# Kernel optimization log

Hardware: AMD Instinct MI355X
Metric: run time of the kernel (lower is better)

Reference implementation:

```python
import jax, jax.numpy as jnp
import numpy as np

DIM = 1024
HEADS = 16
HEAD_DIM = DIM // HEADS
SCALE = HEAD_DIM ** -0.5
EPS = 1e-5


def _ln(x, g, b):
    m = jnp.mean(x, axis=-1, keepdims=True)
    v = jnp.mean((x - m) ** 2, axis=-1, keepdims=True)
    return (x - m) * jax.lax.rsqrt(v + EPS) * g + b


def setup_inputs() -> dict:
    key = jax.random.key(0)
    ks = jax.random.split(key, 12)
    B, N, C = 4, 1024, DIM
    s = lambda fan: 1.0 / np.sqrt(fan)
    return {
        "src_q": jax.random.normal(ks[0], (B, N, C), jnp.float32),
        "src_kv": jax.random.normal(ks[1], (B, N, C), jnp.float32),
        "gq": jnp.ones((C,), jnp.float32), "bq": jnp.zeros((C,), jnp.float32),
        "gkv": jnp.ones((C,), jnp.float32), "bkv": jnp.zeros((C,), jnp.float32),
        "Wq": jax.random.normal(ks[2], (C, C), jnp.float32) * s(C),
        "Wkv": jax.random.normal(ks[3], (C, 2 * C), jnp.float32) * s(C),
        "Wproj": jax.random.normal(ks[4], (C, C), jnp.float32) * s(C),
        "bproj": jnp.zeros((C,), jnp.float32),
        "gn": jnp.ones((C,), jnp.float32), "bn": jnp.zeros((C,), jnp.float32),
        "W1": jax.random.normal(ks[5], (C, 4 * C), jnp.float32) * s(C),
        "b1": jnp.zeros((4 * C,), jnp.float32),
        "W2": jax.random.normal(ks[6], (4 * C, C), jnp.float32) * s(4 * C),
        "b2": jnp.zeros((C,), jnp.float32),
    }


def reference(src_q, src_kv, gq, bq, gkv, bkv, Wq, Wkv, Wproj, bproj,
              gn, bn, W1, b1, W2, b2):
    B, N, C = src_q.shape
    qn = _ln(src_q, gq, bq)
    kvn = _ln(src_kv, gkv, bkv)
    # Q: [B, H, N, d]
    Q = (qn @ Wq).reshape(B, N, HEADS, HEAD_DIM).transpose(0, 2, 1, 3)
    KV = (kvn @ Wkv).reshape(B, N, 2, HEADS, HEAD_DIM).transpose(2, 0, 3, 1, 4)
    K, V = KV[0], KV[1]
    attn = jnp.einsum('bhqd,bhkd->bhqk', Q, K) * SCALE
    attn = jax.nn.softmax(attn, axis=-1)
    # NOTE: original code multiplies by scale a second time here (faithful)
    x = jnp.einsum('bhqk,bhkd->bhqd', attn, V) * SCALE
    x = x.transpose(0, 2, 1, 3).reshape(B, N, C)
    x = x @ Wproj + bproj
    src = src_q + x               # residual (drop_path = identity in eval)
    src = _ln(src, gn, bn)
    h = jax.nn.gelu(src @ W1 + b1, approximate=False)
    src2 = h @ W2 + b2
    return src + src2
```

## Files before the change

### kernel.cpp

```cpp
#include <hip/hip_runtime.h>
#include <hip/hip_bf16.h>
#include <math.h>

typedef __bf16 bf16;
typedef __bf16 bf16x2 __attribute__((ext_vector_type(2)));
typedef __bf16 bf16x8 __attribute__((ext_vector_type(8)));
typedef float f32x4 __attribute__((ext_vector_type(4)));
typedef float f32x16 __attribute__((ext_vector_type(16)));
typedef unsigned int u32;
typedef unsigned int u32x2 __attribute__((ext_vector_type(2)));
typedef unsigned int u32x4 __attribute__((ext_vector_type(4)));

#define SCALE 0.125f

#define GLOAD_LDS16(gptr, lptr)                                      \
  __builtin_amdgcn_global_load_lds(                                  \
      (const __attribute__((address_space(1))) void*)(gptr),         \
      (__attribute__((address_space(3))) void*)(lptr), 16, 0, 0)

template <int N>
__device__ __forceinline__ void vmcnt_wait() {
  if constexpr (N == 0) asm volatile("s_waitcnt vmcnt(0)" ::: "memory");
  else if constexpr (N == 4) asm volatile("s_waitcnt vmcnt(4)" ::: "memory");
  else if constexpr (N == 6) asm volatile("s_waitcnt vmcnt(6)" ::: "memory");
  else static_assert(N == 0 || N == 4 || N == 6, "unsupported vmcnt");
}

__device__ __forceinline__ u32 pk_bf16(float lo, float hi) {
  bf16x2 t;
  t[0] = (bf16)lo;
  t[1] = (bf16)hi;
  return __builtin_bit_cast(u32, t);
}

__device__ __forceinline__ void plane32_swap(u32& a, u32& b) {
  asm volatile("v_permlane32_swap_b32 %0, %1" : "+v"(a), "+v"(b));
}

__global__ __launch_bounds__(256) void ln_f32(const float* __restrict__ x,
                                              const float* __restrict__ g,
                                              const float* __restrict__ b,
                                              bf16* __restrict__ y) {
  long base = (long)blockIdx.x * 1024;
  int tid = threadIdx.x;
  float v[4];
#pragma unroll
  for (int i = 0; i < 4; i++) v[i] = x[base + tid + i * 256];
  float s1 = v[0] + v[1] + v[2] + v[3];
  float s2 = v[0] * v[0] + v[1] * v[1] + v[2] * v[2] + v[3] * v[3];
#pragma unroll
  for (int off = 32; off; off >>= 1) {
    s1 += __shfl_xor(s1, off);
    s2 += __shfl_xor(s2, off);
  }
  __shared__ float aux[2][4];
  int wave = tid >> 6, lane = tid & 63;
  if (lane == 0) { aux[0][wave] = s1; aux[1][wave] = s2; }
  __syncthreads();
  float S1 = aux[0][0] + aux[0][1] + aux[0][2] + aux[0][3];
  float S2 = aux[1][0] + aux[1][1] + aux[1][2] + aux[1][3];
  float mean = S1 * (1.0f / 1024.0f);
  float var = S2 * (1.0f / 1024.0f) - mean * mean;
  float rs = rsqrtf(var + 1e-5f);
#pragma unroll
  for (int i = 0; i < 4; i++) {
    int c = tid + i * 256;
    y[base + c] = (bf16)(((v[i] - mean) * rs) * g[c] + b[c]);
  }
}

__global__ __launch_bounds__(256) void transpose_w(const float* __restrict__ W,
                                                   bf16* __restrict__ Wt,
                                                   int K, int N) {
  __shared__ bf16 tile[64][66];
  int n0 = blockIdx.x * 64, k0 = blockIdx.y * 64;
  int c = threadIdx.x & 63, r4 = threadIdx.x >> 6;
#pragma unroll
  for (int i = 0; i < 16; i++)
    tile[i * 4 + r4][c] = (bf16)W[(long)(k0 + i * 4 + r4) * N + n0 + c];
  __syncthreads();
#pragma unroll
  for (int i = 0; i < 16; i++)
    Wt[(long)(n0 + i * 4 + r4) * K + k0 + c] = tile[c][i * 4 + r4];
}

__global__ __launch_bounds__(256) void extract_vt(const bf16* __restrict__ KV,
                                                  bf16* __restrict__ Vt) {
  __shared__ bf16 tile[64][66];
  int bh = blockIdx.z, b = bh >> 4, h = bh & 15;
  const bf16* src = KV + (long)b * 1024 * 2048 + 1024 + h * 64;
  bf16* dst = Vt + (long)bh * 64 * 1024;
  int n0 = blockIdx.x * 64;
  int c = threadIdx.x & 63, r4 = threadIdx.x >> 6;
#pragma unroll
  for (int i = 0; i < 16; i++)
    tile[i * 4 + r4][c] = src[(long)(n0 + i * 4 + r4) * 2048 + c];
  __syncthreads();
#pragma unroll
  for (int i = 0; i < 16; i++)
    dst[(long)(i * 4 + r4) * 1024 + n0 + c] = tile[c][i * 4 + r4];
}

__global__ __launch_bounds__(256) void attn_fused(
    const bf16* __restrict__ Q,
    const bf16* __restrict__ KV,
    const bf16* __restrict__ Vt,
    bf16* __restrict__ X) {
  __shared__ __align__(16) bf16 Qs[128 * 64];
  __shared__ __align__(16) bf16 Ks[2][64 * 128];
  __shared__ __align__(16) bf16 Vs[2][64 * 128];
  int tid = threadIdx.x, wave = tid >> 6, lane = tid & 63;
  int l31 = lane & 31, h = lane >> 5;
  int bh = blockIdx.y, b = bh >> 4, hd = bh & 15;
  const bf16* Qb = Q + (long)b * 1048576 + hd * 64;
  const bf16* Kb = KV + (long)b * 2097152 + hd * 64;
  const bf16* Vb = Vt + (long)bh * 65536;
  bf16* Xb = X + (long)b * 1048576 + hd * 64;
  int q0 = blockIdx.x * 128;

  const bf16* gk[4];
  const bf16* gv[4];
  int eoKV[4];
#pragma unroll
  for (int t = 0; t < 4; t++) {
    int eo = (t * 256 + tid) * 8;
    eoKV[t] = eo;
    int r2 = eo >> 7, pp = (eo & 127) >> 3, q = pp ^ (r2 & 15);
    gk[t] = &Kb[(long)(r2 + ((q >> 3) << 6)) * 2048 + ((q & 7) << 3)];
    gv[t] = &Vb[(long)r2 * 1024 + (q << 3)];
  }

#pragma unroll
  for (int t = 0; t < 4; t++) {
    int eo = (t * 256 + tid) * 8;
    int r = eo >> 6, p = (eo & 63) >> 3;
    int c = (p ^ (r & 7)) << 3;
    GLOAD_LDS16(&Qb[(long)(q0 + r) * 1024 + c], &Qs[eo]);
  }
#pragma unroll
  for (int t = 0; t < 4; t++) GLOAD_LDS16(gk[t], &Ks[0][eoKV[t]]);
#pragma unroll
  for (int t = 0; t < 4; t++) GLOAD_LDS16(gv[t], &Vs[0][eoKV[t]]);
  __syncthreads();

  bf16x8 qf[4];
  {
    int r = wave * 32 + l31;
#pragma unroll
    for (int dw = 0; dw < 4; dw++) {
      int p = (dw * 2 + h) ^ (r & 7);
      qf[dw] = *(const bf16x8*)&Qs[r * 64 + p * 8];
    }
  }

  const float C = 0.18033688011112042f;
  float m_run = -1e30f, l_run = 0.0f;
  f32x16 acc[2] = {};
  int cur = 0;

  for (int kc = 0; kc < 8; kc++) {
    if (kc < 7) {
#pragma unroll
      for (int t = 0; t < 4; t++)
        GLOAD_LDS16(gk[t] + (long)(kc + 1) * 128 * 2048, &Ks[cur ^ 1][eoKV[t]]);
#pragma unroll
      for (int t = 0; t < 4; t++)
        GLOAD_LDS16(gv[t] + (kc + 1) * 128, &Vs[cur ^ 1][eoKV[t]]);
    }
    const bf16* ks = Ks[cur];
    const bf16* vs = Vs[cur];

    f32x16 s[4] = {};
#pragma unroll
    for (int kt = 0; kt < 4; kt++) {
      int k = kt * 32 + l31;
      int r2 = k & 63, hi = k >> 6;
#pragma unroll
      for (int dw = 0; dw < 4; dw++) {
        int p = (hi * 8 + dw * 2 + h) ^ (r2 & 15);
        bf16x8 kf = *(const bf16x8*)&ks[r2 * 128 + p * 8];
        s[kt] = __builtin_amdgcn_mfma_f32_32x32x16_bf16(kf, qf[dw], s[kt], 0, 0, 0);
      }
    }

    float mk[4];
#pragma unroll
    for (int kt = 0; kt < 4; kt++) {
      float m01 = fmaxf(fmaxf(s[kt][0], s[kt][1]), fmaxf(s[kt][2], s[kt][3]));
      float m23 = fmaxf(fmaxf(s[kt][4], s[kt][5]), fmaxf(s[kt][6], s[kt][7]));
      float m45 = fmaxf(fmaxf(s[kt][8], s[kt][9]), fmaxf(s[kt][10], s[kt][11]));
      float m67 = fmaxf(fmaxf(s[kt][12], s[kt][13]), fmaxf(s[kt][14], s[kt][15]));
      mk[kt] = fmaxf(fmaxf(m01, m23), fmaxf(m45, m67));
    }
    float mx = fmaxf(fmaxf(mk[0], mk[1]), fmaxf(mk[2], mk[3]));
    mx = fmaxf(mx, __shfl_xor(mx, 32));
    float m_new = fmaxf(m_run, mx);
    float alpha = exp2f((m_run - m_new) * C);
    m_run = m_new;
    float mc = m_new * C;
    float rk[4];
#pragma unroll
    for (int kt = 0; kt < 4; kt++) {
      float r0 = 0.0f;
#pragma unroll
      for (int r = 0; r < 16; r++) {
        float pv = exp2f(s[kt][r] * C - mc);
        s[kt][r] = pv;
        r0 += pv;
      }
      rk[kt] = r0;
    }
    float rs = (rk[0] + rk[1]) + (rk[2] + rk[3]);
    rs += __shfl_xor(rs, 32);
    l_run = l_run * alpha + rs;
#pragma unroll
    for (int nt = 0; nt < 2; nt++)
#pragma unroll
      for (int r = 0; r < 16; r++) acc[nt][r] *= alpha;

#pragma unroll
    for (int kw = 0; kw < 8; kw++) {
      int kt = kw >> 1, rb = (kw & 1) * 8;
      u32 wA = pk_bf16(s[kt][rb + 0], s[kt][rb + 1]);
      u32 wB = pk_bf16(s[kt][rb + 2], s[kt][rb + 3]);
      u32 wC = pk_bf16(s[kt][rb + 4], s[kt][rb + 5]);
      u32 wD = pk_bf16(s[kt][rb + 6], s[kt][rb + 7]);
      plane32_swap(wA, wC);
      plane32_swap(wB, wD);
      u32x4 wv = {wA, wB, wC, wD};
      bf16x8 pf = __builtin_bit_cast(bf16x8, wv);
#pragma unroll
      for (int nt = 0; nt < 2; nt++) {
        int r2 = nt * 32 + l31;
        int p = (kw * 2 + h) ^ (r2 & 15);
        bf16x8 vf = *(const bf16x8*)&vs[r2 * 128 + p * 8];
        acc[nt] = __builtin_amdgcn_mfma_f32_32x32x16_bf16(vf, pf, acc[nt], 0, 0, 0);
      }
    }

    if (kc < 7) {
      __syncthreads();
      cur ^= 1;
    }
  }

  float fs = SCALE / l_run;
  bf16* Os = Qs;
  int qrow = wave * 32 + l31;
#pragma unroll
  for (int nt = 0; nt < 2; nt++)
#pragma unroll
    for (int g = 0; g < 4; g++) {
      u32 w0 = pk_bf16(acc[nt][g * 4 + 0] * fs, acc[nt][g * 4 + 1] * fs);
      u32 w1 = pk_bf16(acc[nt][g * 4 + 2] * fs, acc[nt][g * 4 + 3] * fs);
      int s8 = nt * 8 + g * 2 + h;
      int phys = s8 ^ (qrow & 15);
      u32x2 wv = {w0, w1};
      *(u32x2*)&Os[qrow * 64 + phys * 4] = wv;
    }
  int rrow = wave * 32 + (lane >> 1);
  int cbase = (lane & 1) * 32;
#pragma unroll
  for (int t2 = 0; t2 < 4; t2++) {
    int s0 = (lane & 1) * 8 + t2 * 2;
    u32x2 a = *(u32x2*)&Os[rrow * 64 + ((s0 ^ (rrow & 15)) * 4)];
    u32x2 bb = *(u32x2*)&Os[rrow * 64 + (((s0 + 1) ^ (rrow & 15)) * 4)];
    u32x4 o4 = {a[0], a[1], bb[0], bb[1]};
    *(u32x4*)&Xb[(long)(q0 + rrow) * 1024 + cbase + t2 * 8] = o4;
  }
}

template <int BM, int BN, int WR, int WC, int PH, int EPI, int CF32, int RBF16>
__global__ __launch_bounds__(512) void gemm_p(
    const bf16* __restrict__ A, int lda,
    const bf16* __restrict__ B, int ldb,
    void* __restrict__ Cv, int ldc, int K,
    const float* __restrict__ bias,
    const void* __restrict__ resv, int ldr) {
  constexpr int MT = BM / (16 * WR);
  constexpr int NT = BN / (16 * WC);
  constexpr int KSP = 2 / PH;
  constexpr int L = (BM + BN) / 64;
  constexpr int LA = BM / 64;
  constexpr int AE = BM * 64;
  constexpr int BUFE = (BM + BN) * 64;
  __shared__ __align__(16) bf16 lds[3 * BUFE];
  int tid = threadIdx.x;
  int wave = tid >> 6, lane = tid & 63;
  int wm = wave / WC, wn = wave % WC;
  int quad = lane >> 4, l16 = lane & 15;
  int m0 = blockIdx.y * BM, n0 = blockIdx.x * BN;

  const bf16* gp[L];
  int lo[L];
#pragma unroll
  for (int i = 0; i < L; i++) {
    if (i < LA) {
      int eo = (i * 512 + tid) * 8;
      int r = eo >> 6, p = (eo & 63) >> 3;
      int c = (p ^ (r & 7)) << 3;
      gp[i] = &A[(long)(m0 + r) * lda + c];
      lo[i] = eo;
    } else {
      int eo = ((i - LA) * 512 + tid) * 8;
      int r = eo >> 6, p = (eo & 63) >> 3;
      int c = (p ^ (r & 7)) << 3;
      gp[i] = &B[(long)(n0 + r) * ldb + c];
      lo[i] = AE + eo;
    }
  }

  int ntk = K >> 6;
#pragma unroll
  for (int i = 0; i < L; i++) GLOAD_LDS16(gp[i], &lds[lo[i]]);
#pragma unroll
  for (int i = 0; i < L; i++) gp[i] += 64;
#pragma unroll
  for (int i = 0; i < L; i++) GLOAD_LDS16(gp[i], &lds[BUFE + lo[i]]);
#pragma unroll
  for (int i = 0; i < L; i++) gp[i] += 64;
  vmcnt_wait<L>();
  asm volatile("" ::: "memory");
  __builtin_amdgcn_s_barrier();

  f32x4 acc[MT][NT] = {};
  int b = 0;
  for (int t = 0; t < ntk; t++) {
    const bf16* Al = &lds[b * BUFE];
    const bf16* Bl = &lds[b * BUFE + AE];
    int b2 = b + 2; if (b2 >= 3) b2 -= 3;
    bool more = (t + 2) < ntk;
#pragma unroll
    for (int ph = 0; ph < PH; ph++) {
      bf16x8 af[KSP][MT], bv[KSP][NT];
#pragma unroll
      for (int k2 = 0; k2 < KSP; k2++) {
        int ks = ph * KSP + k2;
#pragma unroll
        for (int mt = 0; mt < MT; mt++) {
          int row = wm * (BM / WR) + mt * 16 + l16;
          int p = (ks * 4 + quad) ^ (row & 7);
          af[k2][mt] = *(const bf16x8*)&Al[row * 64 + p * 8];
        }
#pragma unroll
        for (int nt = 0; nt < NT; nt++) {
          int row = wn * (BN / WC) + nt * 16 + l16;
          int p = (ks * 4 + quad) ^ (row & 7);
          bv[k2][nt] = *(const bf16x8*)&Bl[row * 64 + p * 8];
        }
      }
      if (more) {
#pragma unroll
        for (int i = ph * L / PH; i < (ph + 1) * L / PH; i++)
          GLOAD_LDS16(gp[i], &lds[b2 * BUFE + lo[i]]);
      }
      if (ph == PH - 1) {
        if (more) vmcnt_wait<L>();
        else vmcnt_wait<0>();
      }
      asm volatile("" ::: "memory");
      __builtin_amdgcn_s_barrier();
      asm volatile("s_waitcnt lgkmcnt(0)" ::: "memory");
      __builtin_amdgcn_sched_barrier(0);
      __builtin_amdgcn_s_setprio(1);
#pragma unroll
      for (int k2 = 0; k2 < KSP; k2++)
#pragma unroll
        for (int mt = 0; mt < MT; mt++)
#pragma unroll
          for (int nt = 0; nt < NT; nt++)
            acc[mt][nt] = __builtin_amdgcn_mfma_f32_16x16x32_bf16(
                af[k2][mt], bv[k2][nt], acc[mt][nt], 0, 0, 0);
      __builtin_amdgcn_s_setprio(0);
      __builtin_amdgcn_sched_barrier(0);
      __builtin_amdgcn_s_barrier();
    }
#pragma unroll
    for (int i = 0; i < L; i++) gp[i] += 64;
    b += 1; if (b == 3) b = 0;
  }

  int gm = m0 + wm * (BM / WR), gn = n0 + wn * (BN / WC);
#pragma unroll
  for (int nt = 0; nt < NT; nt++) {
    int col = gn + nt * 16 + l16;
    float bvb = (EPI != 0) ? bias[col] : 0.0f;
#pragma unroll
    for (int mt = 0; mt < MT; mt++) {
#pragma unroll
      for (int r = 0; r < 4; r++) {
        int row = gm + mt * 16 + quad * 4 + r;
        float v = acc[mt][nt][r] + bvb;
        if (EPI == 2) {
          v = 0.5f * v * (1.0f + erff(v * 0.70710678118654752f));
        } else if (EPI == 1) {
          float rv = RBF16 ? (float)((const bf16*)resv)[(long)row * ldr + col]
                           : ((const float*)resv)[(long)row * ldr + col];
          v += rv;
        }
        if (CF32)
          ((float*)Cv)[(long)row * ldc + col] = v;
        else
          ((bf16*)Cv)[(long)row * ldc + col] = (bf16)v;
      }
    }
  }
}

extern "C" void kernel_launch(void* const* d_in, const int* in_sizes, int n_in,
                              void* d_out, int out_size, void* d_ws, size_t ws_size,
                              hipStream_t stream) {
  const float* src_q  = (const float*)d_in[0];
  const float* src_kv = (const float*)d_in[1];
  const float* gq     = (const float*)d_in[2];
  const float* bq     = (const float*)d_in[3];
  const float* gkv    = (const float*)d_in[4];
  const float* bkv    = (const float*)d_in[5];
  const float* Wq     = (const float*)d_in[6];
  const float* Wkv    = (const float*)d_in[7];
  const float* Wproj  = (const float*)d_in[8];
  const float* bproj  = (const float*)d_in[9];
  const float* gn     = (const float*)d_in[10];
  const float* bn     = (const float*)d_in[11];
  const float* W1     = (const float*)d_in[12];
  const float* b1     = (const float*)d_in[13];
  const float* W2     = (const float*)d_in[14];
  const float* b2     = (const float*)d_in[15];
  float* out = (float*)d_out;

  char* ws = (char*)d_ws;
  const long MB = 1024 * 1024;
  bf16* Wq_t    = (bf16*)(ws + 0 * MB);
  bf16* Wkv_t   = (bf16*)(ws + 2 * MB);
  bf16* Wproj_t = (bf16*)(ws + 6 * MB);
  bf16* W1_t    = (bf16*)(ws + 8 * MB);
  bf16* W2_t    = (bf16*)(ws + 16 * MB);
  bf16* qn      = (bf16*)(ws + 24 * MB);
  bf16* kvn     = (bf16*)(ws + 32 * MB);
  bf16* Qm      = (bf16*)(ws + 40 * MB);
  bf16* KVm     = (bf16*)(ws + 48 * MB);
  bf16* Vt      = (bf16*)(ws + 64 * MB);
  bf16* xbuf    = (bf16*)(ws + 24 * MB);
  float* tbuf   = (float*)(ws + 48 * MB);
  bf16* sbuf    = (bf16*)(ws + 64 * MB);
  bf16* hbuf    = (bf16*)(ws + 72 * MB);

  transpose_w<<<dim3(16, 16), 256, 0, stream>>>(Wq, Wq_t, 1024, 1024);
  transpose_w<<<dim3(32, 16), 256, 0, stream>>>(Wkv, Wkv_t, 1024, 2048);
  transpose_w<<<dim3(16, 16), 256, 0, stream>>>(Wproj, Wproj_t, 1024, 1024);
  transpose_w<<<dim3(64, 16), 256, 0, stream>>>(W1, W1_t, 1024, 4096);
  transpose_w<<<dim3(16, 64), 256, 0, stream>>>(W2, W2_t, 4096, 1024);

  ln_f32<<<4096, 256, 0, stream>>>(src_q, gq, bq, qn);
  ln_f32<<<4096, 256, 0, stream>>>(src_kv, gkv, bkv, kvn);

  gemm_p<128, 128, 2, 4, 1, 0, 0, 0><<<dim3(8, 32), 512, 0, stream>>>(
      qn, 1024, Wq_t, 1024, Qm, 1024, 1024, nullptr, nullptr, 0);
  gemm_p<256, 128, 4, 2, 2, 0, 0, 0><<<dim3(16, 16), 512, 0, stream>>>(
      kvn, 1024, Wkv_t, 1024, KVm, 2048, 1024, nullptr, nullptr, 0);
  extract_vt<<<dim3(16, 1, 64), 256, 0, stream>>>(KVm, Vt);

  attn_fused<<<dim3(8, 64), 256, 0, stream>>>(Qm, KVm, Vt, xbuf);

  gemm_p<128, 128, 2, 4, 1, 1, 1, 0><<<dim3(8, 32), 512, 0, stream>>>(
      xbuf, 1024, Wproj_t, 1024, tbuf, 1024, 1024, bproj, src_q, 1024);
  ln_f32<<<4096, 256, 0, stream>>>(tbuf, gn, bn, sbuf);
  gemm_p<256, 128, 4, 2, 2, 2, 0, 0><<<dim3(32, 16), 512, 0, stream>>>(
      sbuf, 1024, W1_t, 1024, hbuf, 4096, 1024, b1, nullptr, 0);
  gemm_p<128, 128, 2, 4, 1, 1, 1, 1><<<dim3(8, 32), 512, 0, stream>>>(
      hbuf, 4096, W2_t, 4096, out, 1024, 4096, b2, sbuf, 1024);
}
```

Baseline: 372.0 us.

## Restructure GEMM main loop to one barrier per k-tile and drop phase split

Removes the PH template parameter and its two-phase split of each k-tile. Every k-tile now reads both k-slices of fragments from LDS, issues all prefetch loads, runs the MFMAs, and only then waits on vmcnt and hits a single barrier. Before, each tile waited on vmcnt before compute and used two barriers. This cuts barrier count and lets the global-to-LDS prefetch overlap the MFMA block. In exchange, the larger tiles keep more fragment registers live and lose the finer interleaving of loads with compute.

```diff
diff --git a/kernel.cpp b/kernel.cpp
--- a/kernel.cpp
+++ b/kernel.cpp
@@ -270,7 +270,7 @@
   }
 }
 
-template <int BM, int BN, int WR, int WC, int PH, int EPI, int CF32, int RBF16>
+template <int BM, int BN, int WR, int WC, int EPI, int CF32, int RBF16>
 __global__ __launch_bounds__(512) void gemm_p(
     const bf16* __restrict__ A, int lda,
     const bf16* __restrict__ B, int ldb,
@@ -279,7 +279,6 @@
     const void* __restrict__ resv, int ldr) {
   constexpr int MT = BM / (16 * WR);
   constexpr int NT = BN / (16 * WC);
-  constexpr int KSP = 2 / PH;
   constexpr int L = (BM + BN) / 64;
   constexpr int LA = BM / 64;
   constexpr int AE = BM * 64;
@@ -330,49 +329,47 @@
     const bf16* Bl = &lds[b * BUFE + AE];
     int b2 = b + 2; if (b2 >= 3) b2 -= 3;
     bool more = (t + 2) < ntk;
-#pragma unroll
-    for (int ph = 0; ph < PH; ph++) {
-      bf16x8 af[KSP][MT], bv[KSP][NT];
-#pragma unroll
-      for (int k2 = 0; k2 < KSP; k2++) {
-        int ks = ph * KSP + k2;
-#pragma unroll
-        for (int mt = 0; mt < MT; mt++) {
-          int row = wm * (BM / WR) + mt * 16 + l16;
-          int p = (ks * 4 + quad) ^ (row & 7);
-          af[k2][mt] = *(const bf16x8*)&Al[row * 64 + p * 8];
-        }
-#pragma unroll
-        for (int nt = 0; nt < NT; nt++) {
-          int row = wn * (BN / WC) + nt * 16 + l16;
-          int p = (ks * 4 + quad) ^ (row & 7);
-          bv[k2][nt] = *(const bf16x8*)&Bl[row * 64 + p * 8];
-        }
-      }
-      if (more) {
-#pragma unroll
-        for (int i = ph * L / PH; i < (ph + 1) * L / PH; i++)
-          GLOAD_LDS16(gp[i], &lds[b2 * BUFE + lo[i]]);
-      }
-      if (ph == PH - 1) {
-        if (more) vmcnt_wait<L>();
-        else vmcnt_wait<0>();
-      }
+
+    bf16x8 af[2][MT], bv[2][NT];
+#pragma unroll
+    for (int ks = 0; ks < 2; ks++) {
+#pragma unroll
+      for (int mt = 0; mt < MT; mt++) {
+        int row = wm * (BM / WR) + mt * 16 + l16;
+        int p = (ks * 4 + quad) ^ (row & 7);
+        af[ks][mt] = *(const bf16x8*)&Al[row * 64 + p * 8];
+      }
+#pragma unroll
+      for (int nt = 0; nt < NT; nt++) {
+        int row = wn * (BN / WC) + nt * 16 + l16;
+        int p = (ks * 4 + quad) ^ (row & 7);
+        bv[ks][nt] = *(const bf16x8*)&Bl[row * 64 + p * 8];
+      }
+    }
+    if (more) {
+#pragma unroll
+      for (int i = 0; i < L; i++) GLOAD_LDS16(gp[i], &lds[b2 * BUFE + lo[i]]);
+    }
+    asm volatile("s_waitcnt lgkmcnt(0)" ::: "memory");
+    __builtin_amdgcn_sched_barrier(0);
+    __builtin_amdgcn_s_setprio(1);
+#pragma unroll
+    for (int ks = 0; ks < 2; ks++)
+#pragma unroll
+      for (int mt = 0; mt < MT; mt++)
+#pragma unroll
+        for (int nt = 0; nt < NT; nt++)
+          acc[mt][nt] = __builtin_amdgcn_mfma_f32_16x16x32_bf16(
+              af[ks][mt], bv[ks][nt], acc[mt][nt], 0, 0, 0);
+    __builtin_amdgcn_s_setprio(0);
+    __builtin_amdgcn_sched_barrier(0);
+    if (more) {
+      vmcnt_wait<L>();
+    } else if (t + 1 < ntk) {
+      vmcnt_wait<0>();
+    }
+    if (t + 1 < ntk) {
       asm volatile("" ::: "memory");
-      __builtin_amdgcn_s_barrier();
-      asm volatile("s_waitcnt lgkmcnt(0)" ::: "memory");
-      __builtin_amdgcn_sched_barrier(0);
-      __builtin_amdgcn_s_setprio(1);
-#pragma unroll
-      for (int k2 = 0; k2 < KSP; k2++)
-#pragma unroll
-        for (int mt = 0; mt < MT; mt++)
-#pragma unroll
-          for (int nt = 0; nt < NT; nt++)
-            acc[mt][nt] = __builtin_amdgcn_mfma_f32_16x16x32_bf16(
-                af[k2][mt], bv[k2][nt], acc[mt][nt], 0, 0, 0);
-      __builtin_amdgcn_s_setprio(0);
-      __builtin_amdgcn_sched_barrier(0);
       __builtin_amdgcn_s_barrier();
     }
 #pragma unroll
@@ -454,19 +451,19 @@
   ln_f32<<<4096, 256, 0, stream>>>(src_q, gq, bq, qn);
   ln_f32<<<4096, 256, 0, stream>>>(src_kv, gkv, bkv, kvn);
 
-  gemm_p<128, 128, 2, 4, 1, 0, 0, 0><<<dim3(8, 32), 512, 0, stream>>>(
+  gemm_p<128, 128, 2, 4, 0, 0, 0><<<dim3(8, 32), 512, 0, stream>>>(
       qn, 1024, Wq_t, 1024, Qm, 1024, 1024, nullptr, nullptr, 0);
-  gemm_p<256, 128, 4, 2, 2, 0, 0, 0><<<dim3(16, 16), 512, 0, stream>>>(
+  gemm_p<256, 128, 4, 2, 0, 0, 0><<<dim3(16, 16), 512, 0, stream>>>(
       kvn, 1024, Wkv_t, 1024, KVm, 2048, 1024, nullptr, nullptr, 0);
   extract_vt<<<dim3(16, 1, 64), 256, 0, stream>>>(KVm, Vt);
 
   attn_fused<<<dim3(8, 64), 256, 0, stream>>>(Qm, KVm, Vt, xbuf);
 
-  gemm_p<128, 128, 2, 4, 1, 1, 1, 0><<<dim3(8, 32), 512, 0, stream>>>(
+  gemm_p<128, 128, 2, 4, 1, 1, 0><<<dim3(8, 32), 512, 0, stream>>>(
       xbuf, 1024, Wproj_t, 1024, tbuf, 1024, 1024, bproj, src_q, 1024);
   ln_f32<<<4096, 256, 0, stream>>>(tbuf, gn, bn, sbuf);
-  gemm_p<256, 128, 4, 2, 2, 2, 0, 0><<<dim3(32, 16), 512, 0, stream>>>(
+  gemm_p<256, 128, 4, 2, 2, 0, 0><<<dim3(32, 16), 512, 0, stream>>>(
       sbuf, 1024, W1_t, 1024, hbuf, 4096, 1024, b1, nullptr, 0);
-  gemm_p<128, 128, 2, 4, 1, 1, 1, 1><<<dim3(8, 32), 512, 0, stream>>>(
+  gemm_p<128, 128, 2, 4, 1, 1, 1><<<dim3(8, 32), 512, 0, stream>>>(
       hbuf, 4096, W2_t, 4096, out, 1024, 4096, b2, sbuf, 1024);
 }
```

Measured after the change: 368.4 us. About the same (-1.0%).
